# Optimization experiments

Measured on AMD Instinct MI355X. Metric: run time of the kernel, lower is better.

## Reference

```python
import jax, jax.numpy as jnp
import numpy as np

NUM_GRAPHS = 64
NEG_SLOPE = 0.2  # DGL GATConv default negative_slope


def _gat_layer(h, W, a_l, a_r, b, src, dst, n_nodes):
    # DGL GATConv, num_heads=1: feat = h @ W (no bias in fc),
    # e_ij = LeakyReLU(a_l . feat_src + a_r . feat_dst), softmax over incoming
    # edges of each dst node, out_dst = sum alpha * feat_src + bias.
    feat = h @ W                      # [N, D]
    el = feat @ a_l                   # [N]
    er = feat @ a_r                   # [N]
    e = jax.nn.leaky_relu(el[src] + er[dst], NEG_SLOPE)   # [E]
    m = jax.ops.segment_max(e, dst, num_segments=n_nodes)  # per-dst max
    ex = jnp.exp(e - m[dst])
    s = jax.ops.segment_sum(ex, dst, num_segments=n_nodes)
    alpha = ex / s[dst]               # edge softmax
    out = jax.ops.segment_sum(feat[src] * alpha[:, None], dst, num_segments=n_nodes)
    return out + b


def setup_inputs() -> dict:
    key = jax.random.key(0)
    ks = jax.random.split(key, 12)
    N, E, D_IN, D_H, C = 100000, 1600000, 128, 128, 2
    h = jax.random.normal(ks[0], (N, D_IN), dtype=jnp.float32)
    src = jax.random.randint(ks[1], (E,), 0, N)
    dst = jax.random.randint(ks[2], (E,), 0, N)
    graph_id = jnp.sort(jax.random.randint(ks[3], (N,), 0, NUM_GRAPHS))
    sc = 1.0 / np.sqrt(D_IN)
    params = {
        'W1': jax.random.normal(ks[4], (D_IN, D_H), dtype=jnp.float32) * sc,
        'al1': jax.random.normal(ks[5], (D_H,), dtype=jnp.float32) * sc,
        'ar1': jax.random.normal(ks[6], (D_H,), dtype=jnp.float32) * sc,
        'b1': jnp.zeros((D_H,), dtype=jnp.float32),
        'W2': jax.random.normal(ks[7], (D_H, D_H), dtype=jnp.float32) * sc,
        'al2': jax.random.normal(ks[8], (D_H,), dtype=jnp.float32) * sc,
        'ar2': jax.random.normal(ks[9], (D_H,), dtype=jnp.float32) * sc,
        'b2': jnp.zeros((D_H,), dtype=jnp.float32),
        'Wfc': jax.random.normal(ks[10], (D_H, C), dtype=jnp.float32) * sc,
        'bfc': jnp.zeros((C,), dtype=jnp.float32),
    }
    return dict(h=h, src=src, dst=dst, graph_id=graph_id, **params)


def reference(h, src, dst, graph_id, W1, al1, ar1, b1, W2, al2, ar2, b2, Wfc, bfc):
    n_nodes = h.shape[0]
    x = jax.nn.relu(_gat_layer(h, W1, al1, ar1, b1, src, dst, n_nodes))
    x = jax.nn.relu(_gat_layer(x, W2, al2, ar2, b2, src, dst, n_nodes))
    # dgl.mean_nodes over the batched graph
    counts = jax.ops.segment_sum(jnp.ones((n_nodes,), x.dtype), graph_id,
                                 num_segments=NUM_GRAPHS)
    hg = jax.ops.segment_sum(x, graph_id, num_segments=NUM_GRAPHS)
    hg = hg / jnp.clip(counts, 1.0)[:, None]          # [G, D]
    logits = hg @ Wfc + bfc                            # [G, C]
    return jax.nn.log_softmax(logits, axis=-1)
```

## Files before the change

### kernel.cpp

```cpp
#include <hip/hip_runtime.h>
#include <math.h>

#define NUM_GRAPHS 64
#define D 128
#define PCHUNK 16
#define MT 64
#define ETILE 4096

typedef __attribute__((ext_vector_type(8))) short bf16x8;
typedef __attribute__((ext_vector_type(4))) float f32x4;

__device__ __forceinline__ unsigned bf16rne(float x) {
    unsigned u = __float_as_uint(x);
    return (u + 0x7fffu + ((u >> 16) & 1u)) >> 16;
}
__device__ __forceinline__ float bflo(unsigned u) { return __uint_as_float(u << 16); }
__device__ __forceinline__ float bfhi(unsigned u) { return __uint_as_float(u & 0xffff0000u); }


__global__ __launch_bounds__(256) void k_bucket_hist(const int* __restrict__ dst,
                                                     int* __restrict__ bhist, int E) {
    __shared__ int h[1024];
    int tid = threadIdx.x;
    for (int i = tid; i < 1024; i += 256) h[i] = 0;
    __syncthreads();
    int e0 = blockIdx.x * ETILE;
    int e1 = min(e0 + ETILE, E);
    for (int i = e0 + tid; i < e1; i += 256) atomicAdd(&h[dst[i] >> 7], 1);
    __syncthreads();
    for (int i = tid; i < 1024; i += 256)
        if (h[i]) atomicAdd(&bhist[i], h[i]);
}

__global__ __launch_bounds__(1024) void k_bucket_scan(const int* __restrict__ bhist,
                                                      int* __restrict__ bbase,
                                                      int* __restrict__ bcur,
                                                      int NB, int E,
                                                      int* __restrict__ row_ptr, int N) {
    __shared__ int sm[1024];
    int t = threadIdx.x;
    int v = (t < NB) ? bhist[t] : 0;
    sm[t] = v;
    __syncthreads();
    for (int off = 1; off < 1024; off <<= 1) {
        int y = (t >= off) ? sm[t - off] : 0;
        __syncthreads();
        sm[t] += y;
        __syncthreads();
    }
    if (t < NB) { bbase[t] = sm[t] - v; bcur[t] = sm[t] - v; }
    if (t == 0) { bbase[NB] = E; row_ptr[N] = E; }
}

__global__ __launch_bounds__(256) void k_partition(const int* __restrict__ src,
                                                   const int* __restrict__ dst,
                                                   int* __restrict__ bcur,
                                                   unsigned* __restrict__ part, int E) {
    __shared__ int h[1024];
    __shared__ int cur[1024];
    int tid = threadIdx.x;
    for (int i = tid; i < 1024; i += 256) h[i] = 0;
    __syncthreads();
    int e0 = blockIdx.x * ETILE;
    int e1 = min(e0 + ETILE, E);
    for (int i = e0 + tid; i < e1; i += 256) atomicAdd(&h[dst[i] >> 7], 1);
    __syncthreads();
    for (int i = tid; i < 1024; i += 256) {
        int c = h[i];
        cur[i] = c ? atomicAdd(&bcur[i], c) : 0;
    }
    __syncthreads();
    for (int i = e0 + tid; i < e1; i += 256) {
        int d = dst[i];
        int b = d >> 7;
        int pos = atomicAdd(&cur[b], 1);
        part[pos] = (unsigned)src[i] | ((unsigned)(d & 127) << 17);
    }
}


__global__ void k_prep_w(const float* __restrict__ W1, const float* __restrict__ W2,
                         unsigned short* __restrict__ Wt1, unsigned short* __restrict__ Wt2) {
    const float* W = blockIdx.y ? W2 : W1;
    unsigned short* Wt = blockIdx.y ? Wt2 : Wt1;
    int n = blockIdx.x * 16 + (threadIdx.x >> 4);
    int c = threadIdx.x & 15;
    unsigned v[8];
    #pragma unroll
    for (int j = 0; j < 8; ++j) v[j] = bf16rne(W[(c * 8 + j) * D + n]);
    uint4 pk;
    pk.x = v[0] | (v[1] << 16);
    pk.y = v[2] | (v[3] << 16);
    pk.z = v[4] | (v[5] << 16);
    pk.w = v[6] | (v[7] << 16);
    ((uint4*)Wt)[n * 16 + c] = pk;
}


__global__ __launch_bounds__(256) void k_gemm_mfma_sort(
    const void* __restrict__ Xv, int x_fp32,
    const unsigned short* __restrict__ Wt16,
    const float* __restrict__ al, const float* __restrict__ ar,
    unsigned short* __restrict__ feat16, float* __restrict__ el,
    float* __restrict__ er, float* __restrict__ blockmax, int N, int gemmBlocks,
    const unsigned* __restrict__ part, const int* __restrict__ bbase,
    int* __restrict__ row_ptr, int* __restrict__ csr_src) {
    __shared__ uint4 WsU[128 * 16];
    __shared__ uint4 XsU[MT * 16];
    __shared__ float smax[4];
    int bx = blockIdx.x;
    int T = gridDim.x;
    int g0 = (int)((long long)bx * gemmBlocks / T);
    int g1 = (int)((long long)(bx + 1) * gemmBlocks / T);
    int tid = threadIdx.x;

    if (g1 == g0) {
        int b = bx - g0;
        int base = bbase[b];
        int bcnt = bbase[b + 1] - base;
        int* ldeg = (int*)XsU;
        int* lcur = ldeg + 128;
        if (tid < 128) ldeg[tid] = 0;
        __syncthreads();
        for (int i = tid; i < bcnt; i += 256)
            atomicAdd(&ldeg[part[base + i] >> 17], 1);
        __syncthreads();
        int myv = (tid < 128) ? ldeg[tid] : 0;
        for (int off = 1; off < 128; off <<= 1) {
            int y = 0;
            if (tid < 128 && tid >= off) y = ldeg[tid - off];
            __syncthreads();
            if (tid < 128) ldeg[tid] += y;
            __syncthreads();
        }
        if (tid < 128) {
            int excl = ldeg[tid] - myv;
            int node = (b << 7) + tid;
            if (node < N) row_ptr[node] = base + excl;
            lcur[tid] = base + excl;
        }
        __syncthreads();
        for (int i = tid; i < bcnt; i += 256) {
            unsigned v = part[base + i];
            int pos = atomicAdd(&lcur[v >> 17], 1);
            csr_src[pos] = (int)(v & 0x1FFFFu);
        }
        return;
    }

    int row0 = g0 * MT;

    for (int idx = tid; idx < 128 * 16; idx += 256) {
        int n = idx >> 4, c = idx & 15;
        WsU[(n << 4) | (c ^ (n & 15))] = ((const uint4*)Wt16)[idx];
    }
    if (x_fp32) {
        const float4* X4 = (const float4*)Xv;
        for (int idx = tid; idx < MT * 16; idx += 256) {
            int n = idx >> 4, c = idx & 15;
            int row = row0 + n;
            uint4 o = make_uint4(0, 0, 0, 0);
            if (row < N) {
                float4 f0 = X4[(size_t)row * 32 + c * 2];
                float4 f1 = X4[(size_t)row * 32 + c * 2 + 1];
                o.x = bf16rne(f0.x) | (bf16rne(f0.y) << 16);
                o.y = bf16rne(f0.z) | (bf16rne(f0.w) << 16);
                o.z = bf16rne(f1.x) | (bf16rne(f1.y) << 16);
                o.w = bf16rne(f1.z) | (bf16rne(f1.w) << 16);
            }
            XsU[(n << 4) | (c ^ (n & 15))] = o;
        }
    } else {
        const uint4* X16 = (const uint4*)Xv;
        for (int idx = tid; idx < MT * 16; idx += 256) {
            int n = idx >> 4, c = idx & 15;
            int row = row0 + n;
            uint4 o = make_uint4(0, 0, 0, 0);
            if (row < N) o = X16[(size_t)row * 16 + c];
            XsU[(n << 4) | (c ^ (n & 15))] = o;
        }
    }
    __syncthreads();

    int lane = tid & 63, w = tid >> 6;
    int quad = lane >> 4, l16 = lane & 15;
    const bf16x8* WsF = (const bf16x8*)WsU;
    const bf16x8* XsF = (const bf16x8*)XsU;
    f32x4 acc[8];
    #pragma unroll
    for (int i = 0; i < 8; ++i) acc[i] = (f32x4){0.f, 0.f, 0.f, 0.f};

    int arow = w * 16 + l16;
    #pragma unroll
    for (int ks = 0; ks < 4; ++ks) {
        int c = ks * 4 + quad;
        bf16x8 A = XsF[(arow << 4) | (c ^ l16)];
        #pragma unroll
        for (int nt = 0; nt < 8; ++nt) {
            bf16x8 B = WsF[((nt * 16 + l16) << 4) | (c ^ l16)];
            acc[nt] = __builtin_amdgcn_mfma_f32_16x16x32_bf16(A, B, acc[nt], 0, 0, 0);
        }
    }

    float alv[8], arv[8];
    #pragma unroll
    for (int nt = 0; nt < 8; ++nt) { alv[nt] = al[nt * 16 + l16]; arv[nt] = ar[nt * 16 + l16]; }
    float lmax = -1e30f;
    #pragma unroll
    for (int r = 0; r < 4; ++r) {
        float pl = 0.f, pr = 0.f;
        #pragma unroll
        for (int nt = 0; nt < 8; ++nt) { pl += acc[nt][r] * alv[nt]; pr += acc[nt][r] * arv[nt]; }
        #pragma unroll
        for (int o = 1; o < 16; o <<= 1) { pl += __shfl_xor(pl, o); pr += __shfl_xor(pr, o); }
        int row = row0 + w * 16 + quad * 4 + r;
        if (l16 == 0 && row < N) { el[row] = pl; er[row] = pr; }
        lmax = fmaxf(lmax, pl);
    }
    lmax = fmaxf(lmax, __shfl_xor(lmax, 16));
    lmax = fmaxf(lmax, __shfl_xor(lmax, 32));
    if (lane == 0) smax[w] = lmax;

    unsigned short* XsS = (unsigned short*)XsU;
    #pragma unroll
    for (int nt = 0; nt < 8; ++nt)
        #pragma unroll
        for (int r = 0; r < 4; ++r) {
            int lrow = w * 16 + quad * 4 + r;
            int col = nt * 16 + l16;
            int ch = col >> 3;
            int sc = ch ^ (lrow & 15);
            XsS[lrow * 128 + sc * 8 + (col & 7)] = (unsigned short)bf16rne(acc[nt][r]);
        }
    __syncthreads();
    if (tid == 0)
        blockmax[g0] = fmaxf(fmaxf(smax[0], smax[1]), fmaxf(smax[2], smax[3]));
    for (int idx = tid; idx < MT * 16; idx += 256) {
        int n = idx >> 4, c = idx & 15;
        int row = row0 + n;
        if (row < N) ((uint4*)feat16)[(size_t)row * 16 + c] = XsU[(n << 4) | (c ^ (n & 15))];
    }
}

__global__ void k_foldmax(const float* __restrict__ blockmax, int n,
                          float* __restrict__ glmax) {
    float m = -1e30f;
    for (int i = threadIdx.x; i < n; i += 256) m = fmaxf(m, blockmax[i]);
    #pragma unroll
    for (int o = 32; o >= 1; o >>= 1) m = fmaxf(m, __shfl_xor(m, o));
    __shared__ float sm[4];
    if ((threadIdx.x & 63) == 0) sm[threadIdx.x >> 6] = m;
    __syncthreads();
    if (threadIdx.x == 0)
        glmax[0] = fmaxf(fmaxf(sm[0], sm[1]), fmaxf(sm[2], sm[3]));
}


__global__ __launch_bounds__(256) void k_aggregate(
    const unsigned short* __restrict__ feat16, const float* __restrict__ el,
    const float* __restrict__ er, const int* __restrict__ row_ptr,
    const int* __restrict__ csr_src, const float* __restrict__ bias,
    const float* __restrict__ glmax, unsigned short* __restrict__ outv, int N) {
    int wid = (blockIdx.x * blockDim.x + threadIdx.x) >> 6;
    int lane = threadIdx.x & 63;
    if (wid >= N) return;
    int beg = row_ptr[wid], end = row_ptr[wid + 1];
    float erd = er[wid];
    float M = glmax[0] + erd;
    M = M >= 0.f ? M : 0.2f * M;

    int qa = lane >> 4, sub = lane & 15;
    const uint4* f16 = (const uint4*)feat16;
    float acc[8] = {};
    float s = 0.f;
    int j = beg + qa;
    for (; j + 4 < end; j += 8) {
        int sn0 = csr_src[j], sn1 = csr_src[j + 4];
        float e0 = el[sn0] + erd; e0 = e0 >= 0.f ? e0 : 0.2f * e0;
        float e1 = el[sn1] + erd; e1 = e1 >= 0.f ? e1 : 0.2f * e1;
        float w0 = __expf(e0 - M);
        float w1 = __expf(e1 - M);
        uint4 q0 = f16[(size_t)sn0 * 16 + sub];
        uint4 q1 = f16[(size_t)sn1 * 16 + sub];
        s += w0 + w1;
        acc[0] += w0 * bflo(q0.x) + w1 * bflo(q1.x);
        acc[1] += w0 * bfhi(q0.x) + w1 * bfhi(q1.x);
        acc[2] += w0 * bflo(q0.y) + w1 * bflo(q1.y);
        acc[3] += w0 * bfhi(q0.y) + w1 * bfhi(q1.y);
        acc[4] += w0 * bflo(q0.z) + w1 * bflo(q1.z);
        acc[5] += w0 * bfhi(q0.z) + w1 * bfhi(q1.z);
        acc[6] += w0 * bflo(q0.w) + w1 * bflo(q1.w);
        acc[7] += w0 * bfhi(q0.w) + w1 * bfhi(q1.w);
    }
    if (j < end) {
        int sn = csr_src[j];
        float e = el[sn] + erd; e = e >= 0.f ? e : 0.2f * e;
        float w = __expf(e - M);
        uint4 q = f16[(size_t)sn * 16 + sub];
        s += w;
        acc[0] += w * bflo(q.x); acc[1] += w * bfhi(q.x);
        acc[2] += w * bflo(q.y); acc[3] += w * bfhi(q.y);
        acc[4] += w * bflo(q.z); acc[5] += w * bfhi(q.z);
        acc[6] += w * bflo(q.w); acc[7] += w * bfhi(q.w);
    }
    #pragma unroll
    for (int c = 0; c < 8; ++c) {
        acc[c] += __shfl_xor(acc[c], 16);
        acc[c] += __shfl_xor(acc[c], 32);
    }
    s += __shfl_xor(s, 16);
    s += __shfl_xor(s, 32);
    float inv = (end > beg) ? 1.f / s : 0.f;
    if (lane < 16) {
        float4 b0 = ((const float4*)bias)[lane * 2];
        float4 b1 = ((const float4*)bias)[lane * 2 + 1];
        float v[8];
        v[0] = fmaxf(acc[0] * inv + b0.x, 0.f);
        v[1] = fmaxf(acc[1] * inv + b0.y, 0.f);
        v[2] = fmaxf(acc[2] * inv + b0.z, 0.f);
        v[3] = fmaxf(acc[3] * inv + b0.w, 0.f);
        v[4] = fmaxf(acc[4] * inv + b1.x, 0.f);
        v[5] = fmaxf(acc[5] * inv + b1.y, 0.f);
        v[6] = fmaxf(acc[6] * inv + b1.z, 0.f);
        v[7] = fmaxf(acc[7] * inv + b1.w, 0.f);
        uint4 pk;
        pk.x = bf16rne(v[0]) | (bf16rne(v[1]) << 16);
        pk.y = bf16rne(v[2]) | (bf16rne(v[3]) << 16);
        pk.z = bf16rne(v[4]) | (bf16rne(v[5]) << 16);
        pk.w = bf16rne(v[6]) | (bf16rne(v[7]) << 16);
        ((uint4*)outv)[(size_t)wid * 16 + lane] = pk;
    }
}


__global__ void k_bounds_sorted(const int* __restrict__ gid, int* __restrict__ gs,
                                int* __restrict__ ge, int N) {
    int n = blockIdx.x * blockDim.x + threadIdx.x;
    if (n >= N) return;
    int g = gid[n];
    if (n == 0 || gid[n - 1] != g) gs[g] = n;
    if (n == N - 1 || gid[n + 1] != g) ge[g] = n;
}

__global__ __launch_bounds__(256) void k_pool_partial(const unsigned short* __restrict__ x,
                                                      const int* __restrict__ gs,
                                                      const int* __restrict__ ge,
                                                      float* __restrict__ hg) {
    int g = blockIdx.x, c = blockIdx.y;
    int start = gs[g], last = ge[g];
    if (start > last) return;
    int sub = threadIdx.x & 15;
    int r   = threadIdx.x >> 4;
    const uint4* x4 = (const uint4*)x;
    float acc[8] = {};
    for (int n = start + c * 16 + r; n <= last; n += PCHUNK * 16) {
        uint4 q = x4[(size_t)n * 16 + sub];
        acc[0] += bflo(q.x); acc[1] += bfhi(q.x);
        acc[2] += bflo(q.y); acc[3] += bfhi(q.y);
        acc[4] += bflo(q.z); acc[5] += bfhi(q.z);
        acc[6] += bflo(q.w); acc[7] += bfhi(q.w);
    }
    __shared__ float sm[256][8];
    #pragma unroll
    for (int k = 0; k < 8; ++k) sm[threadIdx.x][k] = acc[k];
    __syncthreads();
    for (int off = 8; off >= 1; off >>= 1) {
        if (r < off) {
            #pragma unroll
            for (int k = 0; k < 8; ++k)
                sm[threadIdx.x][k] += sm[threadIdx.x + off * 16][k];
        }
        __syncthreads();
    }
    if (r == 0) {
        #pragma unroll
        for (int k = 0; k < 8; ++k)
            atomicAdd(&hg[g * D + sub * 8 + k], sm[sub][k]);
    }
}

__global__ void k_final(const float* __restrict__ hg, const int* __restrict__ gs,
                        const int* __restrict__ ge, const float* __restrict__ Wfc,
                        const float* __restrict__ bfc, float* __restrict__ out) {
    int g = threadIdx.x;
    if (g >= NUM_GRAPHS) return;
    int start = gs[g], last = ge[g];
    float cnt = (start <= last) ? (float)(last - start + 1) : 1.f;
    float ic = 1.f / cnt;
    float l0 = bfc[0], l1 = bfc[1];
    for (int d = 0; d < D; d++) {
        float v = hg[g * D + d] * ic;
        l0 += v * Wfc[2 * d];
        l1 += v * Wfc[2 * d + 1];
    }
    float mm = fmaxf(l0, l1);
    float lse = mm + logf(expf(l0 - mm) + expf(l1 - mm));
    out[2 * g] = l0 - lse;
    out[2 * g + 1] = l1 - lse;
}


extern "C" void kernel_launch(void* const* d_in, const int* in_sizes, int n_in,
                              void* d_out, int out_size, void* d_ws, size_t ws_size,
                              hipStream_t stream) {
    const float* h   = (const float*)d_in[0];
    const int* src   = (const int*)d_in[1];
    const int* dst   = (const int*)d_in[2];
    const int* gid   = (const int*)d_in[3];
    const float* W1  = (const float*)d_in[4];
    const float* al1 = (const float*)d_in[5];
    const float* ar1 = (const float*)d_in[6];
    const float* b1  = (const float*)d_in[7];
    const float* W2  = (const float*)d_in[8];
    const float* al2 = (const float*)d_in[9];
    const float* ar2 = (const float*)d_in[10];
    const float* b2  = (const float*)d_in[11];
    const float* Wfc = (const float*)d_in[12];
    const float* bfc = (const float*)d_in[13];
    float* out = (float*)d_out;

    int N = in_sizes[0] / D;
    int E = in_sizes[1];
    int NB = (N + 127) >> 7;

    char* p = (char*)d_ws;
    unsigned short* feat16  = (unsigned short*)p; p += (size_t)N * D * 2;
    unsigned short* featAgg = (unsigned short*)p; p += (size_t)N * D * 2;
    float* el    = (float*)p; p += (size_t)N * 4;
    float* er    = (float*)p; p += (size_t)N * 4;
    int* row_ptr = (int*)p;   p += (size_t)(N + 4) * 4;
    int* csr_src = (int*)p;   p += (size_t)E * 4;
    unsigned* part = (unsigned*)p; p += (size_t)E * 4;
    int* bhist   = (int*)p;   p += 1028 * 4;
    int* bbase   = (int*)p;   p += 1028 * 4;
    int* bcur    = (int*)p;   p += 1028 * 4;
    int* gs      = (int*)p;   p += NUM_GRAPHS * 4;
    int* ge      = (int*)p;   p += NUM_GRAPHS * 4;
    float* hg    = (float*)p; p += NUM_GRAPHS * D * 4;
    unsigned short* Wt1 = (unsigned short*)p; p += D * D * 2;
    unsigned short* Wt2 = (unsigned short*)p; p += D * D * 2;
    float* blockmax = (float*)p; p += (size_t)((N + MT - 1) / MT + 4) * 4;
    float* glmax = (float*)p; p += 4 * 4;

    int nbN = (N + 255) / 256;
    int nbW = (N * 64 + 255) / 256;
    int nbT = (E + ETILE - 1) / ETILE;
    int gemmB = (N + MT - 1) / MT;

    hipMemsetAsync(bhist, 0, (size_t)NB * 4, stream);
    hipMemsetAsync(gs, 0x7f, NUM_GRAPHS * 4, stream);
    hipMemsetAsync(ge, 0xff, NUM_GRAPHS * 4, stream);
    hipMemsetAsync(hg, 0, NUM_GRAPHS * D * 4, stream);

    k_prep_w<<<dim3(8, 2), 256, 0, stream>>>(W1, W2, Wt1, Wt2);
    k_bucket_hist<<<nbT, 256, 0, stream>>>(dst, bhist, E);
    k_bucket_scan<<<1, 1024, 0, stream>>>(bhist, bbase, bcur, NB, E, row_ptr, N);
    k_partition<<<nbT, 256, 0, stream>>>(src, dst, bcur, part, E);

    k_gemm_mfma_sort<<<gemmB + NB, 256, 0, stream>>>(
        h, 1, Wt1, al1, ar1, feat16, el, er, blockmax, N, gemmB,
        part, bbase, row_ptr, csr_src);
    k_foldmax<<<1, 256, 0, stream>>>(blockmax, gemmB, glmax);
    k_aggregate<<<nbW, 256, 0, stream>>>(feat16, el, er, row_ptr, csr_src,
                                         b1, glmax, featAgg, N);

    k_gemm_mfma_sort<<<gemmB, 256, 0, stream>>>(
        featAgg, 0, Wt2, al2, ar2, feat16, el, er, blockmax, N, gemmB,
        part, bbase, row_ptr, csr_src);
    k_foldmax<<<1, 256, 0, stream>>>(blockmax, gemmB, glmax);
    k_aggregate<<<nbW, 256, 0, stream>>>(feat16, el, er, row_ptr, csr_src,
                                         b2, glmax, featAgg, N);

    k_bounds_sorted<<<nbN, 256, 0, stream>>>(gid, gs, ge, N);
    k_pool_partial<<<dim3(NUM_GRAPHS, PCHUNK), 256, 0, stream>>>(featAgg, gs, ge, hg);
    k_final<<<1, 64, 0, stream>>>(hg, gs, ge, Wfc, bfc, out);
}
```

Measured before the change: 366.5 us.

## Merge front-end kernels, replace max-fold with atomic max, unroll aggregation

Folds the bucket histogram, weight prep and graph-bounds kernels into one launch. The per-block max array plus fold kernel is replaced by an order-preserving-encoded atomicMax into a global word that is zeroed by a single merged memset. The aggregation loop is unrolled to four edges per iteration with packed float2 accumulators and byte-offset addressing. Together these cut kernel launches and memsets and raise memory-level parallelism in the gather, at the cost of more registers and atomic contention on one address.

```diff
diff --git a/kernel.cpp b/kernel.cpp
--- a/kernel.cpp
+++ b/kernel.cpp
@@ -9,6 +9,7 @@
 
 typedef __attribute__((ext_vector_type(8))) short bf16x8;
 typedef __attribute__((ext_vector_type(4))) float f32x4;
+typedef __attribute__((ext_vector_type(2))) float f32x2;
 
 __device__ __forceinline__ unsigned bf16rne(float x) {
     unsigned u = __float_as_uint(x);
@@ -17,19 +18,55 @@
 __device__ __forceinline__ float bflo(unsigned u) { return __uint_as_float(u << 16); }
 __device__ __forceinline__ float bfhi(unsigned u) { return __uint_as_float(u & 0xffff0000u); }
 
-
-__global__ __launch_bounds__(256) void k_bucket_hist(const int* __restrict__ dst,
-                                                     int* __restrict__ bhist, int E) {
+__device__ __forceinline__ unsigned encf(float f) {
+    unsigned u = __float_as_uint(f);
+    return (u & 0x80000000u) ? ~u : (u | 0x80000000u);
+}
+__device__ __forceinline__ float decf(unsigned e) {
+    unsigned u = (e & 0x80000000u) ? (e & 0x7fffffffu) : ~e;
+    return __uint_as_float(u);
+}
+
+
+__global__ __launch_bounds__(256) void k_front(
+    const int* __restrict__ dst, int* __restrict__ bhist, int E, int nbT,
+    const float* __restrict__ W1, const float* __restrict__ W2,
+    unsigned short* __restrict__ Wt1, unsigned short* __restrict__ Wt2,
+    const int* __restrict__ gid, int* __restrict__ gs, int* __restrict__ ge, int N) {
     __shared__ int h[1024];
+    int b = blockIdx.x;
     int tid = threadIdx.x;
-    for (int i = tid; i < 1024; i += 256) h[i] = 0;
-    __syncthreads();
-    int e0 = blockIdx.x * ETILE;
-    int e1 = min(e0 + ETILE, E);
-    for (int i = e0 + tid; i < e1; i += 256) atomicAdd(&h[dst[i] >> 7], 1);
-    __syncthreads();
-    for (int i = tid; i < 1024; i += 256)
-        if (h[i]) atomicAdd(&bhist[i], h[i]);
+    if (b < nbT) {
+        for (int i = tid; i < 1024; i += 256) h[i] = 0;
+        __syncthreads();
+        int e0 = b * ETILE;
+        int e1 = min(e0 + ETILE, E);
+        for (int i = e0 + tid; i < e1; i += 256) atomicAdd(&h[dst[i] >> 7], 1);
+        __syncthreads();
+        for (int i = tid; i < 1024; i += 256)
+            if (h[i]) atomicAdd(&bhist[i], h[i]);
+    } else if (b < nbT + 16) {
+        int bb = b - nbT;
+        const float* W = (bb & 8) ? W2 : W1;
+        unsigned short* Wt = (bb & 8) ? Wt2 : Wt1;
+        int n = (bb & 7) * 16 + (tid >> 4);
+        int c = tid & 15;
+        unsigned v[8];
+        #pragma unroll
+        for (int j = 0; j < 8; ++j) v[j] = bf16rne(W[(c * 8 + j) * D + n]);
+        uint4 pk;
+        pk.x = v[0] | (v[1] << 16);
+        pk.y = v[2] | (v[3] << 16);
+        pk.z = v[4] | (v[5] << 16);
+        pk.w = v[6] | (v[7] << 16);
+        ((uint4*)Wt)[n * 16 + c] = pk;
+    } else {
+        int n = (b - nbT - 16) * 256 + tid;
+        if (n >= N) return;
+        int g = gid[n];
+        if (n == 0 || gid[n - 1] != g) gs[g] = n;
+        if (n == N - 1 || gid[n + 1] != g) ge[g] = n;
+    }
 }
 
 __global__ __launch_bounds__(1024) void k_bucket_scan(const int* __restrict__ bhist,
@@ -79,30 +116,12 @@
 }
 
 
-__global__ void k_prep_w(const float* __restrict__ W1, const float* __restrict__ W2,
-                         unsigned short* __restrict__ Wt1, unsigned short* __restrict__ Wt2) {
-    const float* W = blockIdx.y ? W2 : W1;
-    unsigned short* Wt = blockIdx.y ? Wt2 : Wt1;
-    int n = blockIdx.x * 16 + (threadIdx.x >> 4);
-    int c = threadIdx.x & 15;
-    unsigned v[8];
-    #pragma unroll
-    for (int j = 0; j < 8; ++j) v[j] = bf16rne(W[(c * 8 + j) * D + n]);
-    uint4 pk;
-    pk.x = v[0] | (v[1] << 16);
-    pk.y = v[2] | (v[3] << 16);
-    pk.z = v[4] | (v[5] << 16);
-    pk.w = v[6] | (v[7] << 16);
-    ((uint4*)Wt)[n * 16 + c] = pk;
-}
-
-
 __global__ __launch_bounds__(256) void k_gemm_mfma_sort(
     const void* __restrict__ Xv, int x_fp32,
     const unsigned short* __restrict__ Wt16,
     const float* __restrict__ al, const float* __restrict__ ar,
     unsigned short* __restrict__ feat16, float* __restrict__ el,
-    float* __restrict__ er, float* __restrict__ blockmax, int N, int gemmBlocks,
+    float* __restrict__ er, unsigned* __restrict__ glmax_u, int N, int gemmBlocks,
     const unsigned* __restrict__ part, const int* __restrict__ bbase,
     int* __restrict__ row_ptr, int* __restrict__ csr_src) {
     __shared__ uint4 WsU[128 * 16];
@@ -233,8 +252,10 @@
             XsS[lrow * 128 + sc * 8 + (col & 7)] = (unsigned short)bf16rne(acc[nt][r]);
         }
     __syncthreads();
-    if (tid == 0)
-        blockmax[g0] = fmaxf(fmaxf(smax[0], smax[1]), fmaxf(smax[2], smax[3]));
+    if (tid == 0) {
+        float bm = fmaxf(fmaxf(smax[0], smax[1]), fmaxf(smax[2], smax[3]));
+        atomicMax(glmax_u, encf(bm));
+    }
     for (int idx = tid; idx < MT * 16; idx += 256) {
         int n = idx >> 4, c = idx & 15;
         int row = row0 + n;
@@ -242,71 +263,93 @@
     }
 }
 
-__global__ void k_foldmax(const float* __restrict__ blockmax, int n,
-                          float* __restrict__ glmax) {
-    float m = -1e30f;
-    for (int i = threadIdx.x; i < n; i += 256) m = fmaxf(m, blockmax[i]);
-    #pragma unroll
-    for (int o = 32; o >= 1; o >>= 1) m = fmaxf(m, __shfl_xor(m, o));
-    __shared__ float sm[4];
-    if ((threadIdx.x & 63) == 0) sm[threadIdx.x >> 6] = m;
-    __syncthreads();
-    if (threadIdx.x == 0)
-        glmax[0] = fmaxf(fmaxf(sm[0], sm[1]), fmaxf(sm[2], sm[3]));
-}
-
 
 __global__ __launch_bounds__(256) void k_aggregate(
     const unsigned short* __restrict__ feat16, const float* __restrict__ el,
     const float* __restrict__ er, const int* __restrict__ row_ptr,
     const int* __restrict__ csr_src, const float* __restrict__ bias,
-    const float* __restrict__ glmax, unsigned short* __restrict__ outv, int N) {
+    const unsigned* __restrict__ glmax_u, unsigned short* __restrict__ outv, int N) {
     int wid = (blockIdx.x * blockDim.x + threadIdx.x) >> 6;
     int lane = threadIdx.x & 63;
     if (wid >= N) return;
     int beg = row_ptr[wid], end = row_ptr[wid + 1];
     float erd = er[wid];
-    float M = glmax[0] + erd;
-    M = M >= 0.f ? M : 0.2f * M;
+    float M = decf(glmax_u[0]) + erd;
+    M = fmaxf(M, 0.2f * M);
 
     int qa = lane >> 4, sub = lane & 15;
-    const uint4* f16 = (const uint4*)feat16;
-    float acc[8] = {};
+    const char* fb = (const char*)feat16 + (sub << 4);
+    f32x2 a0 = {0.f, 0.f}, a1 = {0.f, 0.f}, a2 = {0.f, 0.f}, a3 = {0.f, 0.f};
     float s = 0.f;
     int j = beg + qa;
+    for (; j + 12 < end; j += 16) {
+        int sn0 = csr_src[j], sn1 = csr_src[j + 4];
+        int sn2 = csr_src[j + 8], sn3 = csr_src[j + 12];
+        float t0 = el[sn0] + erd, t1 = el[sn1] + erd;
+        float t2 = el[sn2] + erd, t3 = el[sn3] + erd;
+        uint4 q0 = *(const uint4*)(fb + ((unsigned)sn0 << 8));
+        uint4 q1 = *(const uint4*)(fb + ((unsigned)sn1 << 8));
+        uint4 q2 = *(const uint4*)(fb + ((unsigned)sn2 << 8));
+        uint4 q3 = *(const uint4*)(fb + ((unsigned)sn3 << 8));
+        t0 = fmaxf(t0, 0.2f * t0); t1 = fmaxf(t1, 0.2f * t1);
+        t2 = fmaxf(t2, 0.2f * t2); t3 = fmaxf(t3, 0.2f * t3);
+        float w0 = __expf(t0 - M), w1 = __expf(t1 - M);
+        float w2 = __expf(t2 - M), w3 = __expf(t3 - M);
+        s += (w0 + w1) + (w2 + w3);
+        f32x2 f;
+        f.x = bflo(q0.x); f.y = bfhi(q0.x); a0 += w0 * f;
+        f.x = bflo(q0.y); f.y = bfhi(q0.y); a1 += w0 * f;
+        f.x = bflo(q0.z); f.y = bfhi(q0.z); a2 += w0 * f;
+        f.x = bflo(q0.w); f.y = bfhi(q0.w); a3 += w0 * f;
+        f.x = bflo(q1.x); f.y = bfhi(q1.x); a0 += w1 * f;
+        f.x = bflo(q1.y); f.y = bfhi(q1.y); a1 += w1 * f;
+        f.x = bflo(q1.z); f.y = bfhi(q1.z); a2 += w1 * f;
+        f.x = bflo(q1.w); f.y = bfhi(q1.w); a3 += w1 * f;
+        f.x = bflo(q2.x); f.y = bfhi(q2.x); a0 += w2 * f;
+        f.x = bflo(q2.y); f.y = bfhi(q2.y); a1 += w2 * f;
+        f.x = bflo(q2.z); f.y = bfhi(q2.z); a2 += w2 * f;
+        f.x = bflo(q2.w); f.y = bfhi(q2.w); a3 += w2 * f;
+        f.x = bflo(q3.x); f.y = bfhi(q3.x); a0 += w3 * f;
+        f.x = bflo(q3.y); f.y = bfhi(q3.y); a1 += w3 * f;
+        f.x = bflo(q3.z); f.y = bfhi(q3.z); a2 += w3 * f;
+        f.x = bflo(q3.w); f.y = bfhi(q3.w); a3 += w3 * f;
+    }
     for (; j + 4 < end; j += 8) {
         int sn0 = csr_src[j], sn1 = csr_src[j + 4];
-        float e0 = el[sn0] + erd; e0 = e0 >= 0.f ? e0 : 0.2f * e0;
-        float e1 = el[sn1] + erd; e1 = e1 >= 0.f ? e1 : 0.2f * e1;
-        float w0 = __expf(e0 - M);
-        float w1 = __expf(e1 - M);
-        uint4 q0 = f16[(size_t)sn0 * 16 + sub];
-        uint4 q1 = f16[(size_t)sn1 * 16 + sub];
+        float t0 = el[sn0] + erd, t1 = el[sn1] + erd;
+        uint4 q0 = *(const uint4*)(fb + ((unsigned)sn0 << 8));
+        uint4 q1 = *(const uint4*)(fb + ((unsigned)sn1 << 8));
+        t0 = fmaxf(t0, 0.2f * t0); t1 = fmaxf(t1, 0.2f * t1);
+        float w0 = __expf(t0 - M), w1 = __expf(t1 - M);
         s += w0 + w1;
-        acc[0] += w0 * bflo(q0.x) + w1 * bflo(q1.x);
-        acc[1] += w0 * bfhi(q0.x) + w1 * bfhi(q1.x);
-        acc[2] += w0 * bflo(q0.y) + w1 * bflo(q1.y);
-        acc[3] += w0 * bfhi(q0.y) + w1 * bfhi(q1.y);
-        acc[4] += w0 * bflo(q0.z) + w1 * bflo(q1.z);
-        acc[5] += w0 * bfhi(q0.z) + w1 * bfhi(q1.z);
-        acc[6] += w0 * bflo(q0.w) + w1 * bflo(q1.w);
-        acc[7] += w0 * bfhi(q0.w) + w1 * bfhi(q1.w);
+        f32x2 f;
+        f.x = bflo(q0.x); f.y = bfhi(q0.x); a0 += w0 * f;
+        f.x = bflo(q0.y); f.y = bfhi(q0.y); a1 += w0 * f;
+        f.x = bflo(q0.z); f.y = bfhi(q0.z); a2 += w0 * f;
+        f.x = bflo(q0.w); f.y = bfhi(q0.w); a3 += w0 * f;
+        f.x = bflo(q1.x); f.y = bfhi(q1.x); a0 += w1 * f;
+        f.x = bflo(q1.y); f.y = bfhi(q1.y); a1 += w1 * f;
+        f.x = bflo(q1.z); f.y = bfhi(q1.z); a2 += w1 * f;
+        f.x = bflo(q1.w); f.y = bfhi(q1.w); a3 += w1 * f;
     }
     if (j < end) {
         int sn = csr_src[j];
-        float e = el[sn] + erd; e = e >= 0.f ? e : 0.2f * e;
-        float w = __expf(e - M);
-        uint4 q = f16[(size_t)sn * 16 + sub];
+        float t = el[sn] + erd;
+        uint4 q = *(const uint4*)(fb + ((unsigned)sn << 8));
+        t = fmaxf(t, 0.2f * t);
+        float w = __expf(t - M);
         s += w;
-        acc[0] += w * bflo(q.x); acc[1] += w * bfhi(q.x);
-        acc[2] += w * bflo(q.y); acc[3] += w * bfhi(q.y);
-        acc[4] += w * bflo(q.z); acc[5] += w * bfhi(q.z);
-        acc[6] += w * bflo(q.w); acc[7] += w * bfhi(q.w);
-    }
+        f32x2 f;
+        f.x = bflo(q.x); f.y = bfhi(q.x); a0 += w * f;
+        f.x = bflo(q.y); f.y = bfhi(q.y); a1 += w * f;
+        f.x = bflo(q.z); f.y = bfhi(q.z); a2 += w * f;
+        f.x = bflo(q.w); f.y = bfhi(q.w); a3 += w * f;
+    }
+    float vr[8] = {a0.x, a0.y, a1.x, a1.y, a2.x, a2.y, a3.x, a3.y};
     #pragma unroll
     for (int c = 0; c < 8; ++c) {
-        acc[c] += __shfl_xor(acc[c], 16);
-        acc[c] += __shfl_xor(acc[c], 32);
+        vr[c] += __shfl_xor(vr[c], 16);
+        vr[c] += __shfl_xor(vr[c], 32);
     }
     s += __shfl_xor(s, 16);
     s += __shfl_xor(s, 32);
@@ -315,14 +358,14 @@
         float4 b0 = ((const float4*)bias)[lane * 2];
         float4 b1 = ((const float4*)bias)[lane * 2 + 1];
         float v[8];
-        v[0] = fmaxf(acc[0] * inv + b0.x, 0.f);
-        v[1] = fmaxf(acc[1] * inv + b0.y, 0.f);
-        v[2] = fmaxf(acc[2] * inv + b0.z, 0.f);
-        v[3] = fmaxf(acc[3] * inv + b0.w, 0.f);
-        v[4] = fmaxf(acc[4] * inv + b1.x, 0.f);
-        v[5] = fmaxf(acc[5] * inv + b1.y, 0.f);
-        v[6] = fmaxf(acc[6] * inv + b1.z, 0.f);
-        v[7] = fmaxf(acc[7] * inv + b1.w, 0.f);
+        v[0] = fmaxf(vr[0] * inv + b0.x, 0.f);
+        v[1] = fmaxf(vr[1] * inv + b0.y, 0.f);
+        v[2] = fmaxf(vr[2] * inv + b0.z, 0.f);
+        v[3] = fmaxf(vr[3] * inv + b0.w, 0.f);
+        v[4] = fmaxf(vr[4] * inv + b1.x, 0.f);
+        v[5] = fmaxf(vr[5] * inv + b1.y, 0.f);
+        v[6] = fmaxf(vr[6] * inv + b1.z, 0.f);
+        v[7] = fmaxf(vr[7] * inv + b1.w, 0.f);
         uint4 pk;
         pk.x = bf16rne(v[0]) | (bf16rne(v[1]) << 16);
         pk.y = bf16rne(v[2]) | (bf16rne(v[3]) << 16);
@@ -332,15 +375,6 @@
     }
 }
 
-
-__global__ void k_bounds_sorted(const int* __restrict__ gid, int* __restrict__ gs,
-                                int* __restrict__ ge, int N) {
-    int n = blockIdx.x * blockDim.x + threadIdx.x;
-    if (n >= N) return;
-    int g = gid[n];
-    if (n == 0 || gid[n - 1] != g) gs[g] = n;
-    if (n == N - 1 || gid[n + 1] != g) ge[g] = n;
-}
 
 __global__ __launch_bounds__(256) void k_pool_partial(const unsigned short* __restrict__ x,
                                                       const int* __restrict__ gs,
@@ -432,46 +466,42 @@
     int* csr_src = (int*)p;   p += (size_t)E * 4;
     unsigned* part = (unsigned*)p; p += (size_t)E * 4;
     int* bhist   = (int*)p;   p += 1028 * 4;
+    unsigned* glmaxu = (unsigned*)p; p += 4 * 4;
+    float* hg    = (float*)p; p += NUM_GRAPHS * D * 4;
+    size_t zbytes = (char*)p - (char*)bhist;
     int* bbase   = (int*)p;   p += 1028 * 4;
     int* bcur    = (int*)p;   p += 1028 * 4;
     int* gs      = (int*)p;   p += NUM_GRAPHS * 4;
     int* ge      = (int*)p;   p += NUM_GRAPHS * 4;
-    float* hg    = (float*)p; p += NUM_GRAPHS * D * 4;
     unsigned short* Wt1 = (unsigned short*)p; p += D * D * 2;
     unsigned short* Wt2 = (unsigned short*)p; p += D * D * 2;
-    float* blockmax = (float*)p; p += (size_t)((N + MT - 1) / MT + 4) * 4;
-    float* glmax = (float*)p; p += 4 * 4;
 
     int nbN = (N + 255) / 256;
     int nbW = (N * 64 + 255) / 256;
     int nbT = (E + ETILE - 1) / ETILE;
     int gemmB = (N + MT - 1) / MT;
 
-    hipMemsetAsync(bhist, 0, (size_t)NB * 4, stream);
+    hipMemsetAsync(bhist, 0, zbytes, stream);
     hipMemsetAsync(gs, 0x7f, NUM_GRAPHS * 4, stream);
     hipMemsetAsync(ge, 0xff, NUM_GRAPHS * 4, stream);
-    hipMemsetAsync(hg, 0, NUM_GRAPHS * D * 4, stream);
-
-    k_prep_w<<<dim3(8, 2), 256, 0, stream>>>(W1, W2, Wt1, Wt2);
-    k_bucket_hist<<<nbT, 256, 0, stream>>>(dst, bhist, E);
+
+    k_front<<<nbT + 16 + nbN, 256, 0, stream>>>(dst, bhist, E, nbT,
+                                                W1, W2, Wt1, Wt2, gid, gs, ge, N);
     k_bucket_scan<<<1, 1024, 0, stream>>>(bhist, bbase, bcur, NB, E, row_ptr, N);
     k_partition<<<nbT, 256, 0, stream>>>(src, dst, bcur, part, E);
 
     k_gemm_mfma_sort<<<gemmB + NB, 256, 0, stream>>>(
-        h, 1, Wt1, al1, ar1, feat16, el, er, blockmax, N, gemmB,
+        h, 1, Wt1, al1, ar1, feat16, el, er, glmaxu, N, gemmB,
         part, bbase, row_ptr, csr_src);
-    k_foldmax<<<1, 256, 0, stream>>>(blockmax, gemmB, glmax);
     k_aggregate<<<nbW, 256, 0, stream>>>(feat16, el, er, row_ptr, csr_src,
-                                         b1, glmax, featAgg, N);
+                                         b1, glmaxu, featAgg, N);
 
     k_gemm_mfma_sort<<<gemmB, 256, 0, stream>>>(
-        featAgg, 0, Wt2, al2, ar2, feat16, el, er, blockmax, N, gemmB,
+        featAgg, 0, Wt2, al2, ar2, feat16, el, er, glmaxu + 1, N, gemmB,
         part, bbase, row_ptr, csr_src);
-    k_foldmax<<<1, 256, 0, stream>>>(blockmax, gemmB, glmax);
     k_aggregate<<<nbW, 256, 0, stream>>>(feat16, el, er, row_ptr, csr_src,
-                                         b2, glmax, featAgg, N);
-
-    k_bounds_sorted<<<nbN, 256, 0, stream>>>(gid, gs, ge, N);
+                                         b2, glmaxu + 1, featAgg, N);
+
     k_pool_partial<<<dim3(NUM_GRAPHS, PCHUNK), 256, 0, stream>>>(featAgg, gs, ge, hg);
     k_final<<<1, 64, 0, stream>>>(hg, gs, ge, Wfc, bfc, out);
 }
```

Measured after the change: 355.9 us. 2.9% less time.
